# Kernel tuning notes

Measured on AMD Instinct MI355X. Metric: run time of the kernel, lower is better.

## Reference

```python
import jax, jax.numpy as jnp
import numpy as np
import math

B, W, BINS, H, K = 1, 2048, 1024, 16, 3  # batch, seq (==cropsize), bins, num_bands, kernel


def setup_inputs() -> dict:
    key = jax.random.key(0)
    ks = jax.random.split(key, 7)
    s = 1.0 / math.sqrt(BINS)
    x = jax.random.normal(ks[0], (B, W, BINS), jnp.float32)
    wq = jax.random.normal(ks[1], (BINS, BINS), jnp.float32) * s
    wk = jax.random.normal(ks[2], (BINS, BINS), jnp.float32) * s
    wv = jax.random.normal(ks[3], (BINS, BINS), jnp.float32) * s
    wo = jax.random.normal(ks[4], (BINS, BINS), jnp.float32) * s
    conv_w = jax.random.normal(ks[5], (BINS, 1, K), jnp.float32) * (1.0 / math.sqrt(K))  # depthwise
    er = jax.random.normal(ks[6], (BINS // H, W), jnp.float32)  # relative-position embeddings
    return {"x": x, "wq": wq, "wk": wk, "wv": wv, "wo": wo, "conv_w": conv_w, "er": er}


def _dwconv(x_bwc, w):
    # depthwise Conv1d, 'same' padding (pad=1, k=3). x: [b,w,c], kernel: [c,1,K]
    y = jax.lax.conv_general_dilated(
        x_bwc.transpose(0, 2, 1), w, window_strides=(1,), padding=[(1, 1)],
        feature_group_count=x_bwc.shape[-1], dimension_numbers=("NCH", "OIH", "NCH"))
    return y.transpose(0, 2, 1)


def reference(x, wq, wk, wv, wo, conv_w, er):
    b, w, c = x.shape
    h = H
    d = c // h
    # NOTE: original torch code applies q_conv to q, k AND v (k_conv/v_conv unused).
    q = _dwconv(x @ wq, conv_w).reshape(b, w, h, d).transpose(0, 2, 1, 3)   # [b,h,w,d]
    k = _dwconv(x @ wk, conv_w).reshape(b, w, h, d).transpose(0, 2, 3, 1)   # [b,h,d,w]
    v = _dwconv(x @ wv, conv_w).reshape(b, w, h, d).transpose(0, 2, 1, 3)   # [b,h,w,d]
    # relative-position skewing trick (Music-Transformer style)
    qe = jnp.einsum("bhwd,dr->bhwr", q, er)                                  # [b,h,w,cropsize]
    p = jnp.pad(qe, ((0, 0), (0, 0), (0, 0), (1, 0))).transpose(0, 1, 3, 2)[:, :, 1:, :]  # [b,h,w,w]
    qk = (jnp.einsum("bhwd,bhdk->bhwk", q, k) + p) / math.sqrt(c)
    a = jax.nn.softmax(qk, axis=-1)
    out = jnp.einsum("bhwk,bhkd->bhwd", a, v).transpose(0, 2, 1, 3).reshape(b, w, c)
    return out @ wo
```

## Files before the change

### kernel.cpp

```cpp
#include <hip/hip_runtime.h>
#include <hip/hip_bf16.h>

typedef __attribute__((ext_vector_type(8))) short short8;
typedef __attribute__((ext_vector_type(4))) float floatx4;

__device__ __forceinline__ float bf2f(unsigned short b) {
    union { unsigned int u; float f; } v; v.u = ((unsigned int)b) << 16; return v.f;
}
__device__ __forceinline__ unsigned short f2bf(float f) {
    union { float f; unsigned int u; } v; v.f = f;
    unsigned int r = v.u + 0x7fffu + ((v.u >> 16) & 1u);
    return (unsigned short)(r >> 16);
}
__device__ __forceinline__ unsigned int pk2bf(float a, float b) {
    __hip_bfloat162 h = __float22bfloat162_rn(make_float2(a, b));
    union { __hip_bfloat162 h; unsigned int u; } v; v.h = h; return v.u;
}

union Pack16 { uint4 v[2]; unsigned short u[16]; };
__device__ __forceinline__ void cvt16(const float* __restrict__ src, float s, Pack16& t) {
    float tmp[16];
    *(float4*)&tmp[0]  = ((const float4*)src)[0];
    *(float4*)&tmp[4]  = ((const float4*)src)[1];
    *(float4*)&tmp[8]  = ((const float4*)src)[2];
    *(float4*)&tmp[12] = ((const float4*)src)[3];
#pragma unroll
    for (int i = 0; i < 16; i++) t.u[i] = f2bf(tmp[i] * s);
}

#define MFMA16(a, b, c) __builtin_amdgcn_mfma_f32_16x16x32_bf16((a), (b), (c), 0, 0, 0)

__device__ __forceinline__ void async16(const unsigned short* g, unsigned short* l) {
    __builtin_amdgcn_global_load_lds(
        (__attribute__((address_space(1))) void*)g,
        (__attribute__((address_space(3))) void*)l, 16, 0, 0);
}

__global__ __launch_bounds__(256) void xcvt(
    const float* __restrict__ x, unsigned short* __restrict__ xb)
{
    const size_t i = ((size_t)blockIdx.x * 256 + threadIdx.x) * 8;
    float4 a = *(const float4*)(x + i), b = *(const float4*)(x + i + 4);
    union { uint4 v; unsigned short u[8]; } o;
    o.u[0] = f2bf(a.x); o.u[1] = f2bf(a.y); o.u[2] = f2bf(a.z); o.u[3] = f2bf(a.w);
    o.u[4] = f2bf(b.x); o.u[5] = f2bf(b.y); o.u[6] = f2bf(b.z); o.u[7] = f2bf(b.w);
    *(uint4*)(xb + i) = o.v;
}

template<bool BT_PRE, bool C_F32>
__global__ __launch_bounds__(256) void gemmGL(
    const unsigned short* __restrict__ Abf,
    const void* __restrict__ B0, const void* __restrict__ B1, const void* __restrict__ B2,
    void* __restrict__ C0, void* __restrict__ C1, void* __restrict__ C2,
    int M, int N, int K)
{
    __shared__ __align__(16) unsigned short As[128 * 64];
    __shared__ __align__(16) unsigned short Bs[64 * 64];
    const int tid = threadIdx.x;
    const int sel = blockIdx.x >> 4;
    const int n0  = (blockIdx.x & 15) * 64;
    const int m0  = blockIdx.y * 128;
    const void* Bp = (sel == 0) ? B0 : (sel == 1) ? B1 : B2;
    void*       Cp = (sel == 0) ? C0 : (sel == 1) ? C1 : C2;

    const int wv = tid >> 6, lane = tid & 63;
    const int quad = lane >> 4, l15 = lane & 15;
    const int wm0 = (wv >> 1) * 64, wn0 = (wv & 1) * 32;

    floatx4 acc[4][2] = {};

    for (int k0 = 0; k0 < K; k0 += 64) {
        __syncthreads();
        {
            const int rr = lane >> 3, pp = lane & 7;
#pragma unroll
            for (int j = 0; j < 4; j++) {
                const int r  = (wv * 4 + j) * 8 + rr;
                const int kg = pp ^ rr ^ ((r >> 4) & 3);
                async16(Abf + (size_t)(m0 + r) * K + k0 + kg * 8,
                        &As[(wv * 4 + j) * 512]);
            }
        }
        if (BT_PRE) {
            const int rr = lane >> 3, pp = lane & 7;
#pragma unroll
            for (int j = 0; j < 2; j++) {
                const int r  = (wv * 2 + j) * 8 + rr;
                const int kg = pp ^ rr ^ ((r >> 4) & 3);
                async16((const unsigned short*)Bp + (size_t)(n0 + r) * K + k0 + kg * 8,
                        &Bs[(wv * 2 + j) * 512]);
            }
        } else {
            const int kr = tid >> 2, nb = (tid & 3) * 16;
            float t[16];
            const float* b = (const float*)Bp + (size_t)(k0 + kr) * N + n0 + nb;
#pragma unroll
            for (int i = 0; i < 4; i++) *(float4*)&t[i * 4] = ((const float4*)b)[i];
            const int k3 = kr >> 3, k7 = kr & 7;
#pragma unroll
            for (int j = 0; j < 16; j++) {
                const int n  = nb + j;
                const int pg = k3 ^ (n & 7) ^ ((n >> 4) & 3);
                Bs[n * 64 + pg * 8 + k7] = f2bf(t[j]);
            }
        }
        __syncthreads();

#pragma unroll
        for (int ks = 0; ks < 2; ks++) {
            short8 af[4], bfr[2];
#pragma unroll
            for (int i = 0; i < 4; i++) {
                const int r = wm0 + i * 16 + l15;
                const int p = (ks * 4 + quad) ^ (r & 7) ^ ((r >> 4) & 3);
                af[i] = *(const short8*)&As[r * 64 + p * 8];
            }
#pragma unroll
            for (int i = 0; i < 2; i++) {
                const int r = wn0 + i * 16 + l15;
                const int p = (ks * 4 + quad) ^ (r & 7) ^ ((r >> 4) & 3);
                bfr[i] = *(const short8*)&Bs[r * 64 + p * 8];
            }
#pragma unroll
            for (int mt = 0; mt < 4; mt++)
#pragma unroll
                for (int nt = 0; nt < 2; nt++)
                    acc[mt][nt] = MFMA16(af[mt], bfr[nt], acc[mt][nt]);
        }
    }

#pragma unroll
    for (int mt = 0; mt < 4; mt++)
#pragma unroll
        for (int nt = 0; nt < 2; nt++)
#pragma unroll
            for (int r = 0; r < 4; r++) {
                const int row = m0 + wm0 + mt * 16 + quad * 4 + r;
                const int col = n0 + wn0 + nt * 16 + l15;
                if (C_F32)
                    ((float*)Cp)[(size_t)row * N + col] = acc[mt][nt][r];
                else
                    ((unsigned short*)Cp)[(size_t)row * N + col] = f2bf(acc[mt][nt][r]);
            }
}

__global__ __launch_bounds__(256) void wtrans(
    const float* __restrict__ W, unsigned short* __restrict__ WT, int Kd, int Nd)
{
    __shared__ __align__(16) unsigned short T[64][72];
    const int tid = threadIdx.x;
    const int n0 = blockIdx.x * 64, k0 = blockIdx.y * 64;
    {
        const int kr = tid >> 2, nc = (tid & 3) * 16;
        Pack16 t;
        cvt16(W + (size_t)(k0 + kr) * Nd + n0 + nc, 1.0f, t);
#pragma unroll
        for (int j = 0; j < 16; j++) T[nc + j][kr] = t.u[j];
    }
    __syncthreads();
    {
        const int nr = tid >> 2, kc = (tid & 3) * 16;
        uint4 x0 = *(const uint4*)&T[nr][kc];
        uint4 x1 = *(const uint4*)&T[nr][kc + 8];
        uint4* dst = (uint4*)(WT + (size_t)(n0 + nr) * Kd + k0 + kc);
        dst[0] = x0; dst[1] = x1;
    }
}

__global__ __launch_bounds__(256) void conv_qk(
    const unsigned short* __restrict__ in, const float* __restrict__ cw,
    unsigned short* __restrict__ out)
{
    const int idx = blockIdx.x * 256 + threadIdx.x;
    const int w = idx >> 7, c0 = (idx & 127) * 8;
    union { uint4 v; unsigned short u[8]; } a = {}, b, c = {};
    b.v = *(const uint4*)(in + (size_t)w * 1024 + c0);
    if (w > 0)    a.v = *(const uint4*)(in + (size_t)(w - 1) * 1024 + c0);
    if (w < 2047) c.v = *(const uint4*)(in + (size_t)(w + 1) * 1024 + c0);
    union { uint4 v; unsigned short u[8]; } o;
#pragma unroll
    for (int i = 0; i < 8; i++) {
        const float* k3 = cw + (size_t)(c0 + i) * 3;
        o.u[i] = f2bf(bf2f(a.u[i]) * k3[0] + bf2f(b.u[i]) * k3[1] + bf2f(c.u[i]) * k3[2]);
    }
    *(uint4*)(out + (size_t)w * 1024 + c0) = o.v;
}

__global__ __launch_bounds__(256) void conv_vt(
    const unsigned short* __restrict__ in, const float* __restrict__ cw,
    unsigned short* __restrict__ vT)
{
    __shared__ __align__(16) unsigned short T[64][72];
    const int tid = threadIdx.x;
    const int w0 = blockIdx.x * 64, h = blockIdx.y;
    {
        const int wr = tid >> 2, c4 = (tid & 3) * 16;
        const int cg = h * 64 + c4;
        const int w = w0 + wr;
        union { uint4 v[2]; unsigned short u[16]; } a = {}, b, c = {};
        b.v[0] = *(const uint4*)(in + (size_t)w * 1024 + cg);
        b.v[1] = *(const uint4*)(in + (size_t)w * 1024 + cg + 8);
        if (w > 0) {
            a.v[0] = *(const uint4*)(in + (size_t)(w - 1) * 1024 + cg);
            a.v[1] = *(const uint4*)(in + (size_t)(w - 1) * 1024 + cg + 8);
        }
        if (w < 2047) {
            c.v[0] = *(const uint4*)(in + (size_t)(w + 1) * 1024 + cg);
            c.v[1] = *(const uint4*)(in + (size_t)(w + 1) * 1024 + cg + 8);
        }
#pragma unroll
        for (int i = 0; i < 16; i++) {
            const float* k3 = cw + (size_t)(cg + i) * 3;
            T[c4 + i][wr] = f2bf(bf2f(a.u[i]) * k3[0] + bf2f(b.u[i]) * k3[1] +
                                 bf2f(c.u[i]) * k3[2]);
        }
    }
    __syncthreads();
    {
        const int dr = tid >> 2, w4 = (tid & 3) * 16;
        uint4 x0 = *(const uint4*)&T[dr][w4];
        uint4 x1 = *(const uint4*)&T[dr][w4 + 8];
        uint4* dst = (uint4*)(vT + (size_t)(h * 64 + dr) * 2048 + w0 + w4);
        dst[0] = x0; dst[1] = x1;
    }
}

__global__ __launch_bounds__(256, 2) void attn16(
    const unsigned short* __restrict__ qc, const unsigned short* __restrict__ kc,
    const unsigned short* __restrict__ vT, const float* __restrict__ er,
    unsigned short* __restrict__ outp)
{
    __shared__ __align__(16) unsigned char smem[70720];
    unsigned short* Qp = (unsigned short*)smem;

    const int tid = threadIdx.x;
    const int q0 = blockIdx.x * 64, h = blockIdx.y;
    const int wv = tid >> 6, lane = tid & 63;
    const int quad = lane >> 4, l15 = lane & 15;
    const float sc2 = 0.03125f * 1.44269504f;

    {
        const int m = tid >> 2, c4 = (tid & 3) * 16;
        union { uint4 v[2]; unsigned short u[16]; } t;
        t.v[0] = *(const uint4*)(qc + (size_t)(q0 + m) * 1024 + h * 64 + c4);
        t.v[1] = *(const uint4*)(qc + (size_t)(q0 + m) * 1024 + h * 64 + c4 + 8);
#pragma unroll
        for (int i = 0; i < 16; i++) t.u[i] = f2bf(bf2f(t.u[i]) * sc2);
        *(uint4*)&Qp[m * 136 + c4]     = t.v[0];
        *(uint4*)&Qp[m * 136 + c4 + 8] = t.v[1];
        Pack16 e;
        cvt16(er + (size_t)m * 2048 + q0 + c4, sc2, e);
#pragma unroll
        for (int j = 0; j < 16; j++) Qp[(c4 + j) * 136 + 64 + m] = e.u[j];
    }
    __syncthreads();

    short8 Bq[4][4];
#pragma unroll
    for (int qm = 0; qm < 4; qm++)
#pragma unroll
        for (int ks = 0; ks < 4; ks++)
            Bq[qm][ks] = *(const short8*)&Qp[(qm * 16 + l15) * 136 + ks * 32 + quad * 8];

    unsigned short* Ps = (unsigned short*)(smem + 17408 + wv * 9216);

    floatx4 oacc[4][4] = {};
    float lp[4] = {0.f, 0.f, 0.f, 0.f};

    for (int i = 0; i < 8; i++) {
        const int kt = 4 * i + wv;
        floatx4 s[4][4] = {};
#pragma unroll
        for (int half = 0; half < 2; half++) {
            short8 Af[2][4];
#pragma unroll
            for (int kmh = 0; kmh < 2; kmh++)
#pragma unroll
                for (int ks = 0; ks < 4; ks++) {
                    const int row = kt * 64 + (half * 2 + kmh) * 16 + l15;
                    const unsigned short* src = (ks < 2) ? kc : qc;
                    const int col = h * 64 + (ks & 1) * 32 + quad * 8;
                    Af[kmh][ks] = *(const short8*)(src + (size_t)row * 1024 + col);
                }
#pragma unroll
            for (int ks = 0; ks < 4; ks++)
#pragma unroll
                for (int kmh = 0; kmh < 2; kmh++)
#pragma unroll
                    for (int qm = 0; qm < 4; qm++)
                        s[half * 2 + kmh][qm] =
                            MFMA16(Af[kmh][ks], Bq[qm][ks], s[half * 2 + kmh][qm]);
        }

#pragma unroll
        for (int km = 0; km < 4; km++)
#pragma unroll
            for (int qm = 0; qm < 4; qm++) {
                float p0 = exp2f(s[km][qm][0]);
                float p1 = exp2f(s[km][qm][1]);
                float p2 = exp2f(s[km][qm][2]);
                float p3 = exp2f(s[km][qm][3]);
                lp[qm] += (p0 + p1) + (p2 + p3);
                uint2 w;
                w.x = pk2bf(p0, p1);
                w.y = pk2bf(p2, p3);
                *(uint2*)&Ps[(qm * 16 + l15) * 72 + km * 16 + quad * 4] = w;
            }

#pragma unroll
        for (int ks = 0; ks < 2; ks++) {
            short8 Pa[4], Vb[4];
#pragma unroll
            for (int mt = 0; mt < 4; mt++)
                Pa[mt] = *(const short8*)&Ps[(mt * 16 + l15) * 72 + ks * 32 + quad * 8];
#pragma unroll
            for (int nt = 0; nt < 4; nt++)
                Vb[nt] = *(const short8*)(vT + (size_t)(h * 64 + nt * 16 + l15) * 2048 +
                                          kt * 64 + ks * 32 + quad * 8);
#pragma unroll
            for (int mt = 0; mt < 4; mt++)
#pragma unroll
                for (int nt = 0; nt < 4; nt++)
                    oacc[mt][nt] = MFMA16(Pa[mt], Vb[nt], oacc[mt][nt]);
        }
    }

#pragma unroll
    for (int qm = 0; qm < 4; qm++) {
        lp[qm] += __shfl_xor(lp[qm], 16);
        lp[qm] += __shfl_xor(lp[qm], 32);
    }
    __syncthreads();
    float* OfW = (float*)smem + wv * 4420;
#pragma unroll
    for (int mt = 0; mt < 4; mt++)
#pragma unroll
        for (int nt = 0; nt < 4; nt++) {
            floatx4 o = oacc[mt][nt];
            *(float4*)&OfW[(nt * 16 + l15) * 68 + mt * 16 + quad * 4] =
                make_float4(o[0], o[1], o[2], o[3]);
        }
    if (quad == 0) {
#pragma unroll
        for (int qm = 0; qm < 4; qm++) OfW[64 * 68 + qm * 16 + l15] = lp[qm];
    }
    __syncthreads();

    {
        const int d = wv * 16 + l15;
#pragma unroll
        for (int i4 = 0; i4 < 4; i4++) {
            float4 os = make_float4(0.f, 0.f, 0.f, 0.f);
            float4 ls = make_float4(0.f, 0.f, 0.f, 0.f);
#pragma unroll
            for (int s4 = 0; s4 < 4; s4++) {
                const float* R = (const float*)smem + s4 * 4420;
                float4 t  = *(const float4*)&R[d * 68 + quad * 16 + i4 * 4];
                float4 tl = *(const float4*)&R[64 * 68 + quad * 16 + i4 * 4];
                os.x += t.x;  os.y += t.y;  os.z += t.z;  os.w += t.w;
                ls.x += tl.x; ls.y += tl.y; ls.z += tl.z; ls.w += tl.w;
            }
            const int qb4 = quad * 16 + i4 * 4;
            const size_t colb = (size_t)h * 64 + d;
            outp[(size_t)(q0 + qb4 + 0) * 1024 + colb] = f2bf(os.x / ls.x);
            outp[(size_t)(q0 + qb4 + 1) * 1024 + colb] = f2bf(os.y / ls.y);
            outp[(size_t)(q0 + qb4 + 2) * 1024 + colb] = f2bf(os.z / ls.z);
            outp[(size_t)(q0 + qb4 + 3) * 1024 + colb] = f2bf(os.w / ls.w);
        }
    }
}

extern "C" void kernel_launch(void* const* d_in, const int* in_sizes, int n_in,
                              void* d_out, int out_size, void* d_ws, size_t ws_size,
                              hipStream_t stream)
{
    const float* x  = (const float*)d_in[0];
    const float* wq = (const float*)d_in[1];
    const float* wk = (const float*)d_in[2];
    const float* wv = (const float*)d_in[3];
    const float* wo = (const float*)d_in[4];
    const float* cw = (const float*)d_in[5];
    const float* er = (const float*)d_in[6];
    float* out = (float*)d_out;
    unsigned short* ws = (unsigned short*)d_ws;

    const size_t SZ = (size_t)2048 * 1024;
    unsigned short* A0 = ws;
    unsigned short* A1 = ws + SZ;
    unsigned short* A2 = ws + 2 * SZ;
    unsigned short* A3 = ws + 3 * SZ;

    xcvt<<<1024, 256, 0, stream>>>(x, A3);
    gemmGL<false, false><<<dim3(48, 16), 256, 0, stream>>>(
        A3, wq, wk, wv, A0, A1, A2, 2048, 1024, 1024);
    conv_qk<<<1024, 256, 0, stream>>>(A0, cw, A3);
    conv_qk<<<1024, 256, 0, stream>>>(A1, cw, A0);
    conv_vt<<<dim3(32, 16), 256, 0, stream>>>(A2, cw, A1);
    attn16<<<dim3(32, 16), 256, 0, stream>>>(A3, A0, A1, er, A2);
    wtrans<<<dim3(16, 16), 256, 0, stream>>>(wo, A0, 1024, 1024);
    gemmGL<true, true><<<dim3(16, 16), 256, 0, stream>>>(
        A2, A0, A0, A0, out, out, out, 2048, 1024, 1024);
}
```

Baseline: 190.4 us.

## Pre-transpose QKV weights to bf16 and fuse the three conv kernels

A new batched wtrans3 kernel converts wq/wk/wv to transposed bf16 once, into the output buffer used as scratch. The QKV GEMM can then stream B tiles with async global-to-LDS loads instead of reloading fp32, converting and scatter-writing the weights in every block. The q/k conv and the v conv-transpose launches are merged into one kernel, and later buffers are remapped onto d_out. This adds an extra pass over the weights and relies on careful aliasing of the output buffer before the final GEMM overwrites it.

```diff
diff --git a/kernel.cpp b/kernel.cpp
--- a/kernel.cpp
+++ b/kernel.cpp
@@ -47,10 +47,11 @@
     *(uint4*)(xb + i) = o.v;
 }
 
-template<bool BT_PRE, bool C_F32>
+template<bool C_F32>
 __global__ __launch_bounds__(256) void gemmGL(
     const unsigned short* __restrict__ Abf,
-    const void* __restrict__ B0, const void* __restrict__ B1, const void* __restrict__ B2,
+    const unsigned short* __restrict__ B0, const unsigned short* __restrict__ B1,
+    const unsigned short* __restrict__ B2,
     void* __restrict__ C0, void* __restrict__ C1, void* __restrict__ C2,
     int M, int N, int K)
 {
@@ -60,8 +61,8 @@
     const int sel = blockIdx.x >> 4;
     const int n0  = (blockIdx.x & 15) * 64;
     const int m0  = blockIdx.y * 128;
-    const void* Bp = (sel == 0) ? B0 : (sel == 1) ? B1 : B2;
-    void*       Cp = (sel == 0) ? C0 : (sel == 1) ? C1 : C2;
+    const unsigned short* Bp = (sel == 0) ? B0 : (sel == 1) ? B1 : B2;
+    void*                 Cp = (sel == 0) ? C0 : (sel == 1) ? C1 : C2;
 
     const int wv = tid >> 6, lane = tid & 63;
     const int quad = lane >> 4, l15 = lane & 15;
@@ -81,27 +82,14 @@
                         &As[(wv * 4 + j) * 512]);
             }
         }
-        if (BT_PRE) {
+        {
             const int rr = lane >> 3, pp = lane & 7;
 #pragma unroll
             for (int j = 0; j < 2; j++) {
                 const int r  = (wv * 2 + j) * 8 + rr;
                 const int kg = pp ^ rr ^ ((r >> 4) & 3);
-                async16((const unsigned short*)Bp + (size_t)(n0 + r) * K + k0 + kg * 8,
+                async16(Bp + (size_t)(n0 + r) * K + k0 + kg * 8,
                         &Bs[(wv * 2 + j) * 512]);
-            }
-        } else {
-            const int kr = tid >> 2, nb = (tid & 3) * 16;
-            float t[16];
-            const float* b = (const float*)Bp + (size_t)(k0 + kr) * N + n0 + nb;
-#pragma unroll
-            for (int i = 0; i < 4; i++) *(float4*)&t[i * 4] = ((const float4*)b)[i];
-            const int k3 = kr >> 3, k7 = kr & 7;
-#pragma unroll
-            for (int j = 0; j < 16; j++) {
-                const int n  = nb + j;
-                const int pg = k3 ^ (n & 7) ^ ((n >> 4) & 3);
-                Bs[n * 64 + pg * 8 + k7] = f2bf(t[j]);
             }
         }
         __syncthreads();
@@ -144,16 +132,15 @@
             }
 }
 
-__global__ __launch_bounds__(256) void wtrans(
-    const float* __restrict__ W, unsigned short* __restrict__ WT, int Kd, int Nd)
+__device__ __forceinline__ void wtrans_body(
+    const float* __restrict__ W, unsigned short* __restrict__ WT,
+    int n0, int k0, int tid)
 {
     __shared__ __align__(16) unsigned short T[64][72];
-    const int tid = threadIdx.x;
-    const int n0 = blockIdx.x * 64, k0 = blockIdx.y * 64;
     {
         const int kr = tid >> 2, nc = (tid & 3) * 16;
         Pack16 t;
-        cvt16(W + (size_t)(k0 + kr) * Nd + n0 + nc, 1.0f, t);
+        cvt16(W + (size_t)(k0 + kr) * 1024 + n0 + nc, 1.0f, t);
 #pragma unroll
         for (int j = 0; j < 16; j++) T[nc + j][kr] = t.u[j];
     }
@@ -162,66 +149,86 @@
         const int nr = tid >> 2, kc = (tid & 3) * 16;
         uint4 x0 = *(const uint4*)&T[nr][kc];
         uint4 x1 = *(const uint4*)&T[nr][kc + 8];
-        uint4* dst = (uint4*)(WT + (size_t)(n0 + nr) * Kd + k0 + kc);
+        uint4* dst = (uint4*)(WT + (size_t)(n0 + nr) * 1024 + k0 + kc);
         dst[0] = x0; dst[1] = x1;
     }
 }
 
-__global__ __launch_bounds__(256) void conv_qk(
-    const unsigned short* __restrict__ in, const float* __restrict__ cw,
-    unsigned short* __restrict__ out)
-{
-    const int idx = blockIdx.x * 256 + threadIdx.x;
-    const int w = idx >> 7, c0 = (idx & 127) * 8;
-    union { uint4 v; unsigned short u[8]; } a = {}, b, c = {};
-    b.v = *(const uint4*)(in + (size_t)w * 1024 + c0);
-    if (w > 0)    a.v = *(const uint4*)(in + (size_t)(w - 1) * 1024 + c0);
-    if (w < 2047) c.v = *(const uint4*)(in + (size_t)(w + 1) * 1024 + c0);
-    union { uint4 v; unsigned short u[8]; } o;
-#pragma unroll
-    for (int i = 0; i < 8; i++) {
-        const float* k3 = cw + (size_t)(c0 + i) * 3;
-        o.u[i] = f2bf(bf2f(a.u[i]) * k3[0] + bf2f(b.u[i]) * k3[1] + bf2f(c.u[i]) * k3[2]);
-    }
-    *(uint4*)(out + (size_t)w * 1024 + c0) = o.v;
-}
-
-__global__ __launch_bounds__(256) void conv_vt(
-    const unsigned short* __restrict__ in, const float* __restrict__ cw,
+__global__ __launch_bounds__(256) void wtrans(
+    const float* __restrict__ W, unsigned short* __restrict__ WT)
+{
+    wtrans_body(W, WT, blockIdx.x * 64, blockIdx.y * 64, threadIdx.x);
+}
+
+__global__ __launch_bounds__(256) void wtrans3(
+    const float* __restrict__ W0, const float* __restrict__ W1,
+    const float* __restrict__ W2, unsigned short* __restrict__ WT)
+{
+    const int z = blockIdx.z;
+    const float* W = (z == 0) ? W0 : (z == 1) ? W1 : W2;
+    wtrans_body(W, WT + (size_t)z * 1024 * 1024,
+                blockIdx.x * 64, blockIdx.y * 64, threadIdx.x);
+}
+
+__global__ __launch_bounds__(256) void conv_all(
+    const unsigned short* __restrict__ q_raw, const unsigned short* __restrict__ k_raw,
+    const unsigned short* __restrict__ v_raw, const float* __restrict__ cw,
+    unsigned short* __restrict__ qc, unsigned short* __restrict__ kc,
     unsigned short* __restrict__ vT)
 {
     __shared__ __align__(16) unsigned short T[64][72];
-    const int tid = threadIdx.x;
-    const int w0 = blockIdx.x * 64, h = blockIdx.y;
-    {
-        const int wr = tid >> 2, c4 = (tid & 3) * 16;
-        const int cg = h * 64 + c4;
-        const int w = w0 + wr;
-        union { uint4 v[2]; unsigned short u[16]; } a = {}, b, c = {};
-        b.v[0] = *(const uint4*)(in + (size_t)w * 1024 + cg);
-        b.v[1] = *(const uint4*)(in + (size_t)w * 1024 + cg + 8);
-        if (w > 0) {
-            a.v[0] = *(const uint4*)(in + (size_t)(w - 1) * 1024 + cg);
-            a.v[1] = *(const uint4*)(in + (size_t)(w - 1) * 1024 + cg + 8);
-        }
-        if (w < 2047) {
-            c.v[0] = *(const uint4*)(in + (size_t)(w + 1) * 1024 + cg);
-            c.v[1] = *(const uint4*)(in + (size_t)(w + 1) * 1024 + cg + 8);
-        }
-#pragma unroll
-        for (int i = 0; i < 16; i++) {
-            const float* k3 = cw + (size_t)(cg + i) * 3;
-            T[c4 + i][wr] = f2bf(bf2f(a.u[i]) * k3[0] + bf2f(b.u[i]) * k3[1] +
-                                 bf2f(c.u[i]) * k3[2]);
-        }
-    }
-    __syncthreads();
-    {
-        const int dr = tid >> 2, w4 = (tid & 3) * 16;
-        uint4 x0 = *(const uint4*)&T[dr][w4];
-        uint4 x1 = *(const uint4*)&T[dr][w4 + 8];
-        uint4* dst = (uint4*)(vT + (size_t)(h * 64 + dr) * 2048 + w0 + w4);
-        dst[0] = x0; dst[1] = x1;
+    const int bx = blockIdx.x;
+    if (bx < 2048) {
+        const unsigned short* in  = (bx < 1024) ? q_raw : k_raw;
+        unsigned short*       out = (bx < 1024) ? qc : kc;
+        const int idx = (bx & 1023) * 256 + threadIdx.x;
+        const int w = idx >> 7, c0 = (idx & 127) * 8;
+        union { uint4 v; unsigned short u[8]; } a = {}, b, c = {};
+        b.v = *(const uint4*)(in + (size_t)w * 1024 + c0);
+        if (w > 0)    a.v = *(const uint4*)(in + (size_t)(w - 1) * 1024 + c0);
+        if (w < 2047) c.v = *(const uint4*)(in + (size_t)(w + 1) * 1024 + c0);
+        union { uint4 v; unsigned short u[8]; } o;
+#pragma unroll
+        for (int i = 0; i < 8; i++) {
+            const float* k3 = cw + (size_t)(c0 + i) * 3;
+            o.u[i] = f2bf(bf2f(a.u[i]) * k3[0] + bf2f(b.u[i]) * k3[1] +
+                          bf2f(c.u[i]) * k3[2]);
+        }
+        *(uint4*)(out + (size_t)w * 1024 + c0) = o.v;
+    } else {
+        const int iv = bx - 2048;
+        const int w0 = (iv & 31) * 64, h = iv >> 5;
+        const int tid = threadIdx.x;
+        {
+            const int wr = tid >> 2, c4 = (tid & 3) * 16;
+            const int cg = h * 64 + c4;
+            const int w = w0 + wr;
+            union { uint4 v[2]; unsigned short u[16]; } a = {}, b, c = {};
+            b.v[0] = *(const uint4*)(v_raw + (size_t)w * 1024 + cg);
+            b.v[1] = *(const uint4*)(v_raw + (size_t)w * 1024 + cg + 8);
+            if (w > 0) {
+                a.v[0] = *(const uint4*)(v_raw + (size_t)(w - 1) * 1024 + cg);
+                a.v[1] = *(const uint4*)(v_raw + (size_t)(w - 1) * 1024 + cg + 8);
+            }
+            if (w < 2047) {
+                c.v[0] = *(const uint4*)(v_raw + (size_t)(w + 1) * 1024 + cg);
+                c.v[1] = *(const uint4*)(v_raw + (size_t)(w + 1) * 1024 + cg + 8);
+            }
+#pragma unroll
+            for (int i = 0; i < 16; i++) {
+                const float* k3 = cw + (size_t)(cg + i) * 3;
+                T[c4 + i][wr] = f2bf(bf2f(a.u[i]) * k3[0] + bf2f(b.u[i]) * k3[1] +
+                                     bf2f(c.u[i]) * k3[2]);
+            }
+        }
+        __syncthreads();
+        {
+            const int dr = tid >> 2, w4 = (tid & 3) * 16;
+            uint4 x0 = *(const uint4*)&T[dr][w4];
+            uint4 x1 = *(const uint4*)&T[dr][w4 + 8];
+            uint4* dst = (uint4*)(vT + (size_t)(h * 64 + dr) * 2048 + w0 + w4);
+            dst[0] = x0; dst[1] = x1;
+        }
     }
 }
 
@@ -383,21 +390,23 @@
     const float* er = (const float*)d_in[6];
     float* out = (float*)d_out;
     unsigned short* ws = (unsigned short*)d_ws;
+    unsigned short* ob = (unsigned short*)d_out;
 
     const size_t SZ = (size_t)2048 * 1024;
+    const size_t WT = (size_t)1024 * 1024;
     unsigned short* A0 = ws;
     unsigned short* A1 = ws + SZ;
     unsigned short* A2 = ws + 2 * SZ;
     unsigned short* A3 = ws + 3 * SZ;
 
     xcvt<<<1024, 256, 0, stream>>>(x, A3);
-    gemmGL<false, false><<<dim3(48, 16), 256, 0, stream>>>(
-        A3, wq, wk, wv, A0, A1, A2, 2048, 1024, 1024);
-    conv_qk<<<1024, 256, 0, stream>>>(A0, cw, A3);
-    conv_qk<<<1024, 256, 0, stream>>>(A1, cw, A0);
-    conv_vt<<<dim3(32, 16), 256, 0, stream>>>(A2, cw, A1);
-    attn16<<<dim3(32, 16), 256, 0, stream>>>(A3, A0, A1, er, A2);
-    wtrans<<<dim3(16, 16), 256, 0, stream>>>(wo, A0, 1024, 1024);
-    gemmGL<true, true><<<dim3(16, 16), 256, 0, stream>>>(
+    wtrans3<<<dim3(16, 16, 3), 256, 0, stream>>>(wq, wk, wv, ob);
+    gemmGL<false><<<dim3(48, 16), 256, 0, stream>>>(
+        A3, ob, ob + WT, ob + 2 * WT, A0, A1, A2, 2048, 1024, 1024);
+    conv_all<<<2560, 256, 0, stream>>>(A0, A1, A2, cw,
+                                       A3, ob, ob + 2 * SZ / 2);
+    wtrans<<<dim3(16, 16), 256, 0, stream>>>(wo, A0);
+    attn16<<<dim3(32, 16), 256, 0, stream>>>(A3, ob, ob + SZ, er, A2);
+    gemmGL<true><<<dim3(16, 16), 256, 0, stream>>>(
         A2, A0, A0, A0, out, out, out, 2048, 1024, 1024);
 }
```

New measurement: 179.4 us. 5.8% less time.
